# Optimization experiments

Hardware: AMD Instinct MI355X
Metric: run time of the kernel (lower is better)

Reference implementation:

```python
import jax, jax.numpy as jnp
import numpy as np

N, K, F_IN, F_OUT = 32768, 16, 128, 128
NEG_SLOPE = 0.2  # LeakyReLU slope in original module


def setup_inputs() -> dict:
    key = jax.random.key(0)
    ks = jax.random.split(key, 8)
    nodes = jax.random.normal(ks[0], (N, F_IN), dtype=jnp.float32)
    neighbors = jax.random.normal(ks[1], (N, K, F_IN), dtype=jnp.float32)
    aspects = jax.random.normal(ks[2], (N, K, F_IN), dtype=jnp.float32)
    attention_scores = jax.random.uniform(ks[3], (N, K), dtype=jnp.float32)
    # Parameters (torch.nn.Linear stores weight as [out, in])
    lim_w = float(np.sqrt(6.0 / (F_IN + F_OUT)))  # xavier_uniform
    W = jax.random.uniform(ks[4], (F_OUT, F_IN), minval=-lim_w, maxval=lim_w, dtype=jnp.float32)
    lim_a = float(np.sqrt(6.0 / (2 * F_IN + F_OUT)))
    Wa = jax.random.uniform(ks[5], (F_OUT, 2 * F_IN), minval=-lim_a, maxval=lim_a, dtype=jnp.float32)
    ba = jax.random.uniform(ks[6], (F_OUT,), minval=-0.05, maxval=0.05, dtype=jnp.float32)
    bias = jnp.zeros((F_OUT,), dtype=jnp.float32)
    return {"nodes": nodes, "neighbors": neighbors, "aspects": aspects,
            "attention_scores": attention_scores, "W": W, "Wa": Wa, "ba": ba, "bias": bias}


def reference(nodes, neighbors, aspects, attention_scores, W, Wa, ba, bias):
    # linear_proj (no bias); dropout(p=0.01) treated as eval/identity
    node_proj = nodes @ W.T                                  # [N, F_OUT]
    neigh_proj = jnp.einsum('nkf,of->nko', neighbors, W)     # [N, K, F_OUT]
    asp_proj = jnp.einsum('nkf,of->nko', aspects, W)         # [N, K, F_OUT]
    # aspects_method == 'linear': cat(neigh_proj, asp_proj) then Linear(2F->F)
    cat = jnp.concatenate([neigh_proj, asp_proj], axis=-1)   # [N, K, 2*F_OUT]
    nap = jnp.einsum('nkf,of->nko', cat, Wa) + ba            # [N, K, F_OUT]
    # per-edge: leakyReLU(nap + broadcast target node proj).exp()
    features_per_edge = jnp.exp(jax.nn.leaky_relu(nap + node_proj[:, None, :], NEG_SLOPE))
    # weight by attention score and sum over neighbors (scatter-sum per node)
    out = jnp.sum(features_per_edge * attention_scores[..., None], axis=1)  # [N, F_OUT]
    # skip_concat_bias: concat=True -> view [N, F_OUT], add bias, ELU activation
    return jax.nn.elu(out + bias)
```

## Files before the change

### kernel.cpp

```cpp
#include <hip/hip_runtime.h>
#include <hip/hip_bf16.h>
#include <stdint.h>

typedef short bf16x8 __attribute__((ext_vector_type(8)));
typedef float f32x4  __attribute__((ext_vector_type(4)));
typedef float f32x2  __attribute__((ext_vector_type(2)));

#define NNODES    32768
#define KNB       16
#define FDIM      128
#define KTOT      384
#define NEG_SLOPE 0.2f

static __device__ __forceinline__ unsigned short f2bf(float x) {
  union { float f; unsigned u; } v; v.f = x;
  unsigned r = v.u + 0x7fffu + ((v.u >> 16) & 1u);
  return (unsigned short)(r >> 16);
}

static __device__ __forceinline__ bf16x8 pack8(f32x4 lo, f32x4 hi) {
  union { __hip_bfloat162 h[4]; bf16x8 v; } u;
  u.h[0] = __float22bfloat162_rn(make_float2(lo[0], lo[1]));
  u.h[1] = __float22bfloat162_rn(make_float2(lo[2], lo[3]));
  u.h[2] = __float22bfloat162_rn(make_float2(hi[0], hi[1]));
  u.h[3] = __float22bfloat162_rn(make_float2(hi[2], hi[3]));
  return u.v;
}

__global__ void prep_weights(const float* __restrict__ W,
                             const float* __restrict__ Wa,
                             unsigned short* __restrict__ Bmat) {
  const int o = blockIdx.x;
  const int f = threadIdx.x;
  const float* war = Wa + o * 256;
  float a1 = 0.f, a2 = 0.f;
  #pragma unroll 8
  for (int j = 0; j < 128; ++j) {
    float w = W[j * 128 + f];
    a1 = fmaf(war[j], w, a1);
    a2 = fmaf(war[128 + j], w, a2);
  }
  Bmat[o * KTOT + f]       = f2bf(a1);
  Bmat[o * KTOT + 128 + f] = f2bf(a2);
  Bmat[o * KTOT + 256 + f] = f2bf(W[o * 128 + f]);
}

__global__ void grn_main(const float* __restrict__ nodes,
                         const float* __restrict__ neighbors,
                         const float* __restrict__ aspects,
                         const float* __restrict__ scores,
                         const unsigned short* __restrict__ Bmat,
                         const float* __restrict__ ba,
                         const float* __restrict__ bias,
                         float* __restrict__ out) {
  const int lane = threadIdx.x & 63;
  const int wv   = threadIdx.x >> 6;
  const int quad = lane >> 4;
  const int l16  = lane & 15;
  const int n0   = blockIdx.x * 8 + wv * 2;

  __shared__ float xpose[4][2][FDIM];

  bf16x8 afrag[2][12];
  #pragma unroll
  for (int i = 0; i < 2; ++i) {
    const int n = n0 + i;
    const float* nb = neighbors + ((size_t)n * KNB + l16) * FDIM;
    const float* as = aspects   + ((size_t)n * KNB + l16) * FDIM;
    const float* nd = nodes     + (size_t)n * FDIM;
    #pragma unroll
    for (int h = 0; h < 2; ++h) {
      f32x4 lo[6], hi[6];
      #pragma unroll
      for (int j = 0; j < 6; ++j) {
        const int kc  = h * 6 + j;
        const int seg = kc >> 2;
        const int fo  = (kc & 3) * 32 + quad * 8;
        const float* src = (seg == 0) ? nb + fo : (seg == 1) ? as + fo : nd + fo;
        lo[j] = *(const f32x4*)src;
        hi[j] = *(const f32x4*)(src + 4);
      }
      #pragma unroll
      for (int j = 0; j < 6; ++j) afrag[i][h * 6 + j] = pack8(lo[j], hi[j]);
    }
  }

  f32x4 acc[2][8];
  #pragma unroll
  for (int i = 0; i < 2; ++i)
    #pragma unroll
    for (int ct = 0; ct < 8; ++ct)
      acc[i][ct] = (f32x4){0.f, 0.f, 0.f, 0.f};

  #pragma unroll
  for (int kc = 0; kc < 12; ++kc) {
    const unsigned short* bbase = Bmat + (size_t)l16 * KTOT + kc * 32 + quad * 8;
    #pragma unroll
    for (int ct = 0; ct < 8; ++ct) {
      bf16x8 bfrag = *(const bf16x8*)(bbase + (size_t)(ct * 16) * KTOT);
      acc[0][ct] = __builtin_amdgcn_mfma_f32_16x16x32_bf16(afrag[0][kc], bfrag, acc[0][ct], 0, 0, 0);
      acc[1][ct] = __builtin_amdgcn_mfma_f32_16x16x32_bf16(afrag[1][kc], bfrag, acc[1][ct], 0, 0, 0);
    }
  }

  #pragma unroll
  for (int i = 0; i < 2; ++i) {
    const int n = n0 + i;
    f32x4 sc = *(const f32x4*)(scores + (size_t)n * KNB + quad * 4);
    #pragma unroll
    for (int ct = 0; ct < 8; ++ct) {
      const int c = ct * 16 + l16;
      const float bav = ba[c];
      float s = 0.f;
      #pragma unroll
      for (int r = 0; r < 4; ++r) {
        float t  = acc[i][ct][r] + bav;
        float lr = t > 0.f ? t : NEG_SLOPE * t;
        s = fmaf(__expf(lr), sc[r], s);
      }
      s += __shfl_xor(s, 16);
      s += __shfl_xor(s, 32);
      if ((ct & 3) == quad) xpose[wv][i][c] = s;
    }
  }
  __syncthreads();

  #pragma unroll
  for (int i = 0; i < 2; ++i) {
    f32x2 sv = *(const f32x2*)&xpose[wv][i][2 * lane];
    f32x2 bv = *(const f32x2*)(bias + 2 * lane);
    float v0 = sv[0] + bv[0];
    float v1 = sv[1] + bv[1];
    v0 = v0 > 0.f ? v0 : (__expf(v0) - 1.f);
    v1 = v1 > 0.f ? v1 : (__expf(v1) - 1.f);
    *(f32x2*)(out + (size_t)(n0 + i) * FDIM + 2 * lane) = (f32x2){v0, v1};
  }
}

extern "C" void kernel_launch(void* const* d_in, const int* in_sizes, int n_in,
                              void* d_out, int out_size, void* d_ws, size_t ws_size,
                              hipStream_t stream) {
  const float* nodes     = (const float*)d_in[0];
  const float* neighbors = (const float*)d_in[1];
  const float* aspects   = (const float*)d_in[2];
  const float* scores    = (const float*)d_in[3];
  const float* W         = (const float*)d_in[4];
  const float* Wa        = (const float*)d_in[5];
  const float* ba        = (const float*)d_in[6];
  const float* bias      = (const float*)d_in[7];
  unsigned short* Bmat   = (unsigned short*)d_ws;

  prep_weights<<<128, 128, 0, stream>>>(W, Wa, Bmat);
  grn_main<<<NNODES / 8, 256, 0, stream>>>(nodes, neighbors, aspects, scores,
                                           Bmat, ba, bias, (float*)d_out);
}
```

Measured before the change: 677.8 us.

## Stage neighbor/aspect tiles via global_load_lds DMA and split output columns across waves

Each block now handles 4 nodes. Every wave DMAs one node's neighbor and aspect tiles straight into LDS with global_load_lds, using an XOR-swizzled layout to avoid bank conflicts. Waves then share nodes: each computes 2 nodes by 64 output columns, reading its A fragments from LDS, which halves per-wave B-matrix traffic and removes the LDS transpose before the output write. The aim is to cut register pressure and raise load throughput and occupancy (launch_bounds 256,2), at the cost of 64KB of LDS per block and extra sync and LDS reads.

```diff
diff --git a/kernel.cpp b/kernel.cpp
--- a/kernel.cpp
+++ b/kernel.cpp
@@ -4,13 +4,19 @@
 
 typedef short bf16x8 __attribute__((ext_vector_type(8)));
 typedef float f32x4  __attribute__((ext_vector_type(4)));
-typedef float f32x2  __attribute__((ext_vector_type(2)));
 
 #define NNODES    32768
 #define KNB       16
 #define FDIM      128
 #define KTOT      384
 #define NEG_SLOPE 0.2f
+
+#define AS1 __attribute__((address_space(1)))
+#define AS3 __attribute__((address_space(3)))
+
+static __device__ __forceinline__ void dma16(const void* g, void* lds) {
+  __builtin_amdgcn_global_load_lds((const AS1 void*)g, (AS3 void*)lds, 16, 0, 0);
+}
 
 static __device__ __forceinline__ unsigned short f2bf(float x) {
   union { float f; unsigned u; } v; v.f = x;
@@ -30,8 +36,7 @@
 __global__ void prep_weights(const float* __restrict__ W,
                              const float* __restrict__ Wa,
                              unsigned short* __restrict__ Bmat) {
-  const int o = blockIdx.x;
-  const int f = threadIdx.x;
+  const int o = blockIdx.x, f = threadIdx.x;
   const float* war = Wa + o * 256;
   float a1 = 0.f, a2 = 0.f;
   #pragma unroll 8
@@ -45,95 +50,115 @@
   Bmat[o * KTOT + 256 + f] = f2bf(W[o * 128 + f]);
 }
 
-__global__ void grn_main(const float* __restrict__ nodes,
-                         const float* __restrict__ neighbors,
-                         const float* __restrict__ aspects,
-                         const float* __restrict__ scores,
-                         const unsigned short* __restrict__ Bmat,
-                         const float* __restrict__ ba,
-                         const float* __restrict__ bias,
-                         float* __restrict__ out) {
+__global__ void __launch_bounds__(256, 2)
+grn_main(const float* __restrict__ nodes,
+         const float* __restrict__ neighbors,
+         const float* __restrict__ aspects,
+         const float* __restrict__ scores,
+         const unsigned short* __restrict__ Bmat,
+         const float* __restrict__ ba,
+         const float* __restrict__ bias,
+         float* __restrict__ out) {
   const int lane = threadIdx.x & 63;
   const int wv   = threadIdx.x >> 6;
   const int quad = lane >> 4;
   const int l16  = lane & 15;
-  const int n0   = blockIdx.x * 8 + wv * 2;
+  const int n0   = blockIdx.x * 4;
 
-  __shared__ float xpose[4][2][FDIM];
+  __shared__ float slab_f[4 * 4096];
+  char* slab = (char*)slab_f;
 
-  bf16x8 afrag[2][12];
-  #pragma unroll
-  for (int i = 0; i < 2; ++i) {
-    const int n = n0 + i;
-    const float* nb = neighbors + ((size_t)n * KNB + l16) * FDIM;
-    const float* as = aspects   + ((size_t)n * KNB + l16) * FDIM;
-    const float* nd = nodes     + (size_t)n * FDIM;
+  {
+    const int nw = n0 + wv;
+    const float* tbase[2] = { neighbors + (size_t)nw * KNB * FDIM,
+                              aspects   + (size_t)nw * KNB * FDIM };
+    const int q5 = lane & 31;
+    const int rhalf = lane >> 5;
     #pragma unroll
-    for (int h = 0; h < 2; ++h) {
-      f32x4 lo[6], hi[6];
+    for (int T = 0; T < 2; ++T) {
       #pragma unroll
-      for (int j = 0; j < 6; ++j) {
-        const int kc  = h * 6 + j;
-        const int seg = kc >> 2;
-        const int fo  = (kc & 3) * 32 + quad * 8;
-        const float* src = (seg == 0) ? nb + fo : (seg == 1) ? as + fo : nd + fo;
-        lo[j] = *(const f32x4*)src;
-        hi[j] = *(const f32x4*)(src + 4);
+      for (int j2 = 0; j2 < 8; ++j2) {
+        const int r   = 2 * j2 + rhalf;
+        const int c16 = (q5 & 24) | ((q5 ^ r) & 7);
+        const float* g = tbase[T] + r * FDIM + c16 * 4;
+        dma16(g, slab + (size_t)wv * 16384 + T * 8192 + j2 * 1024);
       }
-      #pragma unroll
-      for (int j = 0; j < 6; ++j) afrag[i][h * 6 + j] = pack8(lo[j], hi[j]);
     }
   }
 
-  f32x4 acc[2][8];
+  const int b = wv & 1, g = wv >> 1;
+  bf16x8 nf[2][4];
+  f32x4  sc[2];
   #pragma unroll
-  for (int i = 0; i < 2; ++i)
+  for (int il = 0; il < 2; ++il) {
+    const int n = n0 + 2 * b + il;
     #pragma unroll
-    for (int ct = 0; ct < 8; ++ct)
-      acc[i][ct] = (f32x4){0.f, 0.f, 0.f, 0.f};
+    for (int kk = 0; kk < 4; ++kk) {
+      const float* src = nodes + (size_t)n * FDIM + kk * 32 + quad * 8;
+      nf[il][kk] = pack8(*(const f32x4*)src, *(const f32x4*)(src + 4));
+    }
+    sc[il] = *(const f32x4*)(scores + (size_t)n * KNB + quad * 4);
+  }
+
+  __syncthreads();
+
+  f32x4 acc[2][4];
+  #pragma unroll
+  for (int il = 0; il < 2; ++il)
+    #pragma unroll
+    for (int t = 0; t < 4; ++t)
+      acc[il][t] = (f32x4){0.f, 0.f, 0.f, 0.f};
+
+  const unsigned short* bb = Bmat + ((size_t)(g * 4) * 16 + l16) * KTOT + quad * 8;
 
   #pragma unroll
   for (int kc = 0; kc < 12; ++kc) {
-    const unsigned short* bbase = Bmat + (size_t)l16 * KTOT + kc * 32 + quad * 8;
+    bf16x8 af[2];
+    if (kc < 8) {
+      const int T = kc >> 2, kcq = kc & 3;
+      #pragma unroll
+      for (int il = 0; il < 2; ++il) {
+        const char* sb = slab + (size_t)(2 * b + il) * 16384 + T * 8192;
+        const int c0 = kcq * 8 + quad * 2;
+        const int u0 = l16 * 32 + ((c0 & 24) | (((c0 + 0) ^ l16) & 7));
+        const int u1 = l16 * 32 + (((c0 + 1) & 24) | (((c0 + 1) ^ l16) & 7));
+        f32x4 lo = *(const f32x4*)(sb + u0 * 16);
+        f32x4 hi = *(const f32x4*)(sb + u1 * 16);
+        af[il] = pack8(lo, hi);
+      }
+    } else {
+      af[0] = nf[0][kc - 8];
+      af[1] = nf[1][kc - 8];
+    }
     #pragma unroll
-    for (int ct = 0; ct < 8; ++ct) {
-      bf16x8 bfrag = *(const bf16x8*)(bbase + (size_t)(ct * 16) * KTOT);
-      acc[0][ct] = __builtin_amdgcn_mfma_f32_16x16x32_bf16(afrag[0][kc], bfrag, acc[0][ct], 0, 0, 0);
-      acc[1][ct] = __builtin_amdgcn_mfma_f32_16x16x32_bf16(afrag[1][kc], bfrag, acc[1][ct], 0, 0, 0);
+    for (int t = 0; t < 4; ++t) {
+      bf16x8 bf = *(const bf16x8*)(bb + (size_t)(t * 16) * KTOT + kc * 32);
+      acc[0][t] = __builtin_amdgcn_mfma_f32_16x16x32_bf16(af[0], bf, acc[0][t], 0, 0, 0);
+      acc[1][t] = __builtin_amdgcn_mfma_f32_16x16x32_bf16(af[1], bf, acc[1][t], 0, 0, 0);
     }
   }
 
   #pragma unroll
-  for (int i = 0; i < 2; ++i) {
-    const int n = n0 + i;
-    f32x4 sc = *(const f32x4*)(scores + (size_t)n * KNB + quad * 4);
+  for (int il = 0; il < 2; ++il) {
+    const int n = n0 + 2 * b + il;
     #pragma unroll
-    for (int ct = 0; ct < 8; ++ct) {
-      const int c = ct * 16 + l16;
+    for (int t = 0; t < 4; ++t) {
+      const int c = (g * 4 + t) * 16 + l16;
       const float bav = ba[c];
       float s = 0.f;
       #pragma unroll
       for (int r = 0; r < 4; ++r) {
-        float t  = acc[i][ct][r] + bav;
-        float lr = t > 0.f ? t : NEG_SLOPE * t;
-        s = fmaf(__expf(lr), sc[r], s);
+        float tt = acc[il][t][r] + bav;
+        float lr = tt > 0.f ? tt : NEG_SLOPE * tt;
+        s = fmaf(__expf(lr), sc[il][r], s);
       }
       s += __shfl_xor(s, 16);
       s += __shfl_xor(s, 32);
-      if ((ct & 3) == quad) xpose[wv][i][c] = s;
+      if (quad == t) {
+        float v = s + bias[c];
+        out[(size_t)n * FDIM + c] = v > 0.f ? v : (__expf(v) - 1.f);
+      }
     }
-  }
-  __syncthreads();
-
-  #pragma unroll
-  for (int i = 0; i < 2; ++i) {
-    f32x2 sv = *(const f32x2*)&xpose[wv][i][2 * lane];
-    f32x2 bv = *(const f32x2*)(bias + 2 * lane);
-    float v0 = sv[0] + bv[0];
-    float v1 = sv[1] + bv[1];
-    v0 = v0 > 0.f ? v0 : (__expf(v0) - 1.f);
-    v1 = v1 > 0.f ? v1 : (__expf(v1) - 1.f);
-    *(f32x2*)(out + (size_t)(n0 + i) * FDIM + 2 * lane) = (f32x2){v0, v1};
   }
 }
 
@@ -151,6 +176,6 @@
   unsigned short* Bmat   = (unsigned short*)d_ws;
 
   prep_weights<<<128, 128, 0, stream>>>(W, Wa, Bmat);
-  grn_main<<<NNODES / 8, 256, 0, stream>>>(nodes, neighbors, aspects, scores,
+  grn_main<<<NNODES / 4, 256, 0, stream>>>(nodes, neighbors, aspects, scores,
                                            Bmat, ba, bias, (float*)d_out);
 }
```

New measurement: 693.0 us. 2.2% more time.
